# Kernel optimization log

Measured on AMD Instinct MI355X. Metric: run time of the kernel, lower is better.

The kernel has to match this reference:

```python
import jax, jax.numpy as jnp
import numpy as np

NA, NW, H = 20000, 100000, 128
DA, DW = 64, 128
E_CR, E_IN, E_CO = 400000, 600000, 300000


def _seg_softmax(logits, seg, n):
    m = jax.ops.segment_max(logits, seg, num_segments=n)
    e = jnp.exp(logits - m[seg])
    s = jax.ops.segment_sum(e, seg, num_segments=n)
    return e / (s[seg] + 1e-16)


def _gat(x_src, x_dst, edge, W, b, a_s, a_d):
    # PyG GATConv, heads=1, concat=False, shared lin for src/dst, add_self_loops=True
    n_src, n_dst = x_src.shape[0], x_dst.shape[0]
    loops = jnp.arange(min(n_src, n_dst), dtype=edge.dtype)
    src = jnp.concatenate([edge[0], loops])
    dst = jnp.concatenate([edge[1], loops])
    hs = x_src @ W            # [n_src, H]
    hd = x_dst @ W            # [n_dst, H]
    logit = jax.nn.leaky_relu((hs @ a_s)[src] + (hd @ a_d)[dst], 0.2)
    alpha = _seg_softmax(logit, dst, n_dst)          # softmax over in-neighborhoods
    out = jax.ops.segment_sum(alpha[:, None] * hs[src], dst, num_segments=n_dst)
    return out + b


def _mlp2(x, w1, b1, w2, b2):
    return jax.nn.relu(x @ w1 + b1) @ w2 + b2


def setup_inputs() -> dict:
    key = jax.random.key(0)
    ks = iter(jax.random.split(key, 40))

    def p(shape, scale=0.1):
        return jax.random.normal(next(ks), shape, jnp.float32) * scale

    def edges(n_src, n_dst, E):
        s = jax.random.randint(next(ks), (E,), 0, n_src, dtype=jnp.int32)
        d = jax.random.randint(next(ks), (E,), 0, n_dst, dtype=jnp.int32)
        d = jnp.where(s == d, (d + 1) % n_dst, d)  # keep input loop-free (PyG strips them)
        return jnp.stack([s, d])

    e_creates = edges(NA, NW, E_CR)
    inp = {
        'artist_feat': jax.random.normal(next(ks), (NA, DA), jnp.float32),
        'work_feat': jax.random.normal(next(ks), (NW, DW), jnp.float32),
        'a_w1': p((DA, H)), 'a_b1': jnp.zeros(H, jnp.float32),
        'a_w2': p((H, H)), 'a_b2': jnp.zeros(H, jnp.float32),
        'w_w1': p((DW, H)), 'w_b1': jnp.zeros(H, jnp.float32),
        'w_w2': p((H, H)), 'w_b2': jnp.zeros(H, jnp.float32),
        'cr_W': p((H, H)), 'cr_b': jnp.zeros(H, jnp.float32), 'cr_as': p((H,)), 'cr_ad': p((H,)),
        'in_W': p((H, H)), 'in_b': jnp.zeros(H, jnp.float32), 'in_as': p((H,)), 'in_ad': p((H,)),
        'co_W': p((H, H)), 'co_b': jnp.zeros(H, jnp.float32), 'co_as': p((H,)), 'co_ad': p((H,)),
        'p_w1': p((2 * H, 256)), 'p_b1': jnp.zeros(256, jnp.float32),
        'p_w2': p((256, 128)), 'p_b2': jnp.zeros(128, jnp.float32),
        'p_w3': p((128, 1)), 'p_b3': jnp.zeros(1, jnp.float32),
        'e_creates': e_creates,
        'e_created_by': jnp.flip(e_creates, axis=0),  # reverse relation [work, artist]
        'e_infl': edges(NW, NW, E_IN),
        'e_collab': edges(NA, NA, E_CO),
    }
    return inp


def reference(artist_feat, work_feat,
              a_w1, a_b1, a_w2, a_b2,
              w_w1, w_b1, w_w2, w_b2,
              cr_W, cr_b, cr_as, cr_ad,
              in_W, in_b, in_as, in_ad,
              co_W, co_b, co_as, co_ad,
              p_w1, p_b1, p_w2, p_b2, p_w3, p_b3,
              e_creates, e_created_by, e_infl, e_collab):
    ax = _mlp2(artist_feat, a_w1, a_b1, a_w2, a_b2)      # [NA, H]
    wx = _mlp2(work_feat, w_w1, w_b1, w_w2, w_b2)        # [NW, H]
    wx = jax.nn.elu(_gat(ax, wx, e_creates, cr_W, cr_b, cr_as, cr_ad))
    wx = jax.nn.elu(_gat(wx, wx, e_infl, in_W, in_b, in_as, in_ad))
    au = _gat(wx, ax, e_created_by, cr_W, cr_b, cr_as, cr_ad)  # no elu (matches source)
    ac = jax.nn.elu(_gat(au, au, e_collab, co_W, co_b, co_as, co_ad))
    comb = jnp.concatenate([au, ac], axis=1)             # [NA, 2H]
    h = jax.nn.relu(comb @ p_w1 + p_b1)                  # dropout is identity in eval
    h = jax.nn.relu(h @ p_w2 + p_b2)
    return (h @ p_w3 + p_b3).squeeze()
```

## Files before the change

### kernel.cpp

```cpp
#include <hip/hip_runtime.h>
#include <hip/hip_bf16.h>
#include <cstddef>

#define NA 20000
#define NW 100000
#define HH 128
#define DA 64
#define E_CR 400000
#define E_IN 600000
#define E_CO 300000

#define ROW1 0
#define ROW2 (NW)
#define ROW3 (2 * NW)
#define ROW4 (2 * NW + NA)
#define NTOT (2 * NW + 2 * NA)
#define CAPW 40
#define CAPA 88
#define NPREP (10 * 128 + 1)
#define GNB ((NA + 127) / 128)

typedef short v8s __attribute__((ext_vector_type(8)));
typedef float v4f __attribute__((ext_vector_type(4)));

constexpr int PSLOT = 2 * 128 * 264;

__device__ inline short f2bf(float x) {
    union { float f; unsigned u; } c; c.f = x;
    unsigned r = c.u + 0x7fff + ((c.u >> 16) & 1);
    return (short)(r >> 16);
}
__device__ inline float bf2f(short s) {
    union { unsigned u; float f; } c; c.u = ((unsigned)(unsigned short)s) << 16;
    return c.f;
}
__device__ inline float bfu2f(unsigned short s) {
    union { unsigned u; float f; } c; c.u = ((unsigned)s) << 16;
    return c.f;
}

__device__ inline void split8(const float* xv, v8s& h, v8s& l) {
#pragma unroll
    for (int p = 0; p < 4; ++p) {
        float2 xf; xf.x = xv[2 * p]; xf.y = xv[2 * p + 1];
        __hip_bfloat162 hb = __float22bfloat162_rn(xf);
        float2 hf = __bfloat1622float2(hb);
        float2 lf; lf.x = xf.x - hf.x; lf.y = xf.y - hf.y;
        __hip_bfloat162 lb = __float22bfloat162_rn(lf);
        union { __hip_bfloat162 b; short2 s; } uh, ul;
        uh.b = hb; ul.b = lb;
        h[2 * p] = uh.s.x; h[2 * p + 1] = uh.s.y;
        l[2 * p] = ul.s.x; l[2 * p + 1] = ul.s.y;
    }
}

struct AppChunk { const int* e; int E; int* pad; int cap; int* deg; };

__device__ inline void do_append(const AppChunk& ap, int bid) {
    int b0 = bid * 1024 + threadIdx.x;
    int s[4], d[4]; bool ok[4];
#pragma unroll
    for (int u = 0; u < 4; ++u) {
        int i = b0 + u * 256;
        ok[u] = i < ap.E;
        s[u] = 0; d[u] = 0;
        if (ok[u]) { s[u] = ap.e[i]; d[u] = ap.e[ap.E + i]; }
    }
    int p[4];
#pragma unroll
    for (int u = 0; u < 4; ++u) if (ok[u]) p[u] = atomicAdd(&ap.deg[d[u]], 1);
#pragma unroll
    for (int u = 0; u < 4; ++u)
        if (ok[u] && p[u] < ap.cap)
            ap.pad[(size_t)d[u] * ap.cap + p[u]] = s[u];
}

struct PrepDesc { const float* src; int ldw; int K; };
struct PrepArgs {
    PrepDesc d[10]; const float* wvW; const float* wvA; float* vd;
    const float* gX; const float* gB; float* gY; int gM;
};

__global__ __launch_bounds__(256) void k_prep_append(PrepArgs a, short* __restrict__ out,
                                                    AppChunk ap)
{
    __shared__ short Bs2[2 * 128 * 72];
    if (blockIdx.x >= NPREP + GNB) { do_append(ap, blockIdx.x - NPREP - GNB); return; }
    if (blockIdx.x >= NPREP) {
        int bid = blockIdx.x - NPREP;
        const int tid = threadIdx.x;
        const int wave = tid >> 6, lane = tid & 63;
        const int l15 = lane & 15, quad = lane >> 4;
        const int wrow = bid * 128 + wave * 32;
        for (int e = tid; e < 64 * 128; e += 256) {
            int n = e & 127, k = e >> 7;
            float x = a.d[0].src[(size_t)k * 128 + n];
            short h = f2bf(x);
            short l = f2bf(x - bf2f(h));
            Bs2[n * 72 + k] = h;
            Bs2[128 * 72 + n * 72 + k] = l;
        }
        v8s ah[2][2], al[2][2];
#pragma unroll
        for (int rf = 0; rf < 2; ++rf) {
            int r = wrow + rf * 16 + l15; if (r >= a.gM) r = a.gM - 1;
            const float* xp = a.gX + (size_t)r * DA + quad * 8;
#pragma unroll
            for (int kf = 0; kf < 2; ++kf) {
                float xv[8];
                *(float4*)&xv[0] = *(const float4*)(xp + kf * 32);
                *(float4*)&xv[4] = *(const float4*)(xp + kf * 32 + 4);
                split8(xv, ah[rf][kf], al[rf][kf]);
            }
        }
        __syncthreads();
        v4f acc[2][8];
#pragma unroll
        for (int rf = 0; rf < 2; ++rf)
#pragma unroll
            for (int cf = 0; cf < 8; ++cf) acc[rf][cf] = (v4f){0.f, 0.f, 0.f, 0.f};
#pragma unroll
        for (int kf = 0; kf < 2; ++kf) {
#pragma unroll
            for (int cf = 0; cf < 8; ++cf) {
                int coff = (cf * 16 + l15) * 72 + kf * 32 + quad * 8;
                v8s bh = *(const v8s*)&Bs2[coff];
                v8s bl = *(const v8s*)&Bs2[128 * 72 + coff];
#pragma unroll
                for (int rf = 0; rf < 2; ++rf) {
                    acc[rf][cf] = __builtin_amdgcn_mfma_f32_16x16x32_bf16(al[rf][kf], bh, acc[rf][cf], 0, 0, 0);
                    acc[rf][cf] = __builtin_amdgcn_mfma_f32_16x16x32_bf16(ah[rf][kf], bl, acc[rf][cf], 0, 0, 0);
                    acc[rf][cf] = __builtin_amdgcn_mfma_f32_16x16x32_bf16(ah[rf][kf], bh, acc[rf][cf], 0, 0, 0);
                }
            }
        }
        float bv[8];
#pragma unroll
        for (int cf = 0; cf < 8; ++cf) bv[cf] = a.gB[cf * 16 + l15];
#pragma unroll
        for (int rf = 0; rf < 2; ++rf) {
#pragma unroll
            for (int reg = 0; reg < 4; ++reg) {
                int r = wrow + rf * 16 + quad * 4 + reg;
                if (r >= a.gM) continue;
                float* yp = a.gY + (size_t)r * HH;
#pragma unroll
                for (int cf = 0; cf < 8; ++cf) {
                    float o = acc[rf][cf][reg] + bv[cf];
                    yp[cf * 16 + l15] = o > 0.f ? o : 0.f;
                }
            }
        }
        return;
    }
    if (blockIdx.x == NPREP - 1) {
        __shared__ float sa[HH];
        int t = threadIdx.x;
        if (t < HH) sa[t] = a.wvA[t];
        __syncthreads();
        if (t < HH) {
            float s = 0.f;
            for (int jj = 0; jj < HH; ++jj) s += a.wvW[(size_t)t * HH + jj] * sa[jj];
            a.vd[t] = s;
        }
        return;
    }
    int m = blockIdx.x >> 7;
    int e = (blockIdx.x & 127) * 256 + threadIdx.x;
    PrepDesc dd = a.d[m];
    int K = dd.K;
    int KP = (K <= 128) ? K + 8 : K;
    if (e >= K * 128) return;
    int n = e & 127, k = e >> 7;
    float x = dd.src[(size_t)k * dd.ldw + n];
    short h = f2bf(x);
    short l = f2bf(x - bf2f(h));
    short* base = out + (size_t)m * PSLOT;
    base[n * KP + k] = h;
    base[128 * KP + n * KP + k] = l;
}

template<int K, int ACT, int NSS, int ST, int LDSB, int OBF, int DUAL, int XBF>
__global__ __launch_bounds__(256, 2) void k_mfma(
    const float* __restrict__ X, int ldx,
    const short* __restrict__ Wp,
    const float* __restrict__ bias,
    float* __restrict__ Y, int ldy, int M,
    const float* __restrict__ v1, float* __restrict__ ss1,
    const float* __restrict__ v2, float* __restrict__ ss2,
    const float* __restrict__ sb)
{
    constexpr int KF = K / 32;
    constexpr int KP = LDSB ? K + 8 : K;
    __shared__ short Bs[LDSB ? 2 * 128 * (K + 8) : 8];
    const int tid = threadIdx.x;
    const int wave = tid >> 6, lane = tid & 63;
    const int l15 = lane & 15, quad = lane >> 4;
    int bid = blockIdx.x;
    if (DUAL) {
        int g0 = gridDim.x >> 1;
        if (bid >= g0) { bid -= g0; Wp += PSLOT; bias += 128; Y += 128; }
    }
    const int wrow = bid * 128 + wave * 32;

    if (LDSB) {
        const float4* src = (const float4*)Wp;
        float4* dst = (float4*)Bs;
        constexpr int total = 2 * 128 * KP / 8;
        for (int i = tid; i < total; i += 256) dst[i] = src[i];
    }

    v4f acc[2][8];
#pragma unroll
    for (int rf = 0; rf < 2; ++rf)
#pragma unroll
        for (int cf = 0; cf < 8; ++cf) acc[rf][cf] = (v4f){0.f, 0.f, 0.f, 0.f};

    v8s ah[2][KF], al[2][KF];
#pragma unroll
    for (int rf = 0; rf < 2; ++rf) {
        int r = wrow + rf * 16 + l15; if (r >= M) r = M - 1;
        if (XBF) {
            const unsigned short* xp = (const unsigned short*)X + (size_t)r * ldx + quad * 8;
#pragma unroll
            for (int kf = 0; kf < KF; ++kf)
                ah[rf][kf] = *(const v8s*)(xp + kf * 32);
        } else {
            const float* xp = X + (size_t)r * ldx + quad * 8;
#pragma unroll
            for (int kf = 0; kf < KF; ++kf) {
                float xv[8];
                *(float4*)&xv[0] = *(const float4*)(xp + kf * 32);
                *(float4*)&xv[4] = *(const float4*)(xp + kf * 32 + 4);
                split8(xv, ah[rf][kf], al[rf][kf]);
            }
        }
    }
    if (LDSB) __syncthreads();
#pragma unroll
    for (int kf = 0; kf < KF; ++kf) {
#pragma unroll
        for (int cf = 0; cf < 8; ++cf) {
            const short* bp = LDSB ? &Bs[(cf * 16 + l15) * KP + kf * 32 + quad * 8]
                                   : Wp + (size_t)(cf * 16 + l15) * K + kf * 32 + quad * 8;
            v8s bh = *(const v8s*)bp;
            v8s bl = *(const v8s*)(bp + 128 * KP);
#pragma unroll
            for (int rf = 0; rf < 2; ++rf) {
                if (!XBF) acc[rf][cf] = __builtin_amdgcn_mfma_f32_16x16x32_bf16(al[rf][kf], bh, acc[rf][cf], 0, 0, 0);
                acc[rf][cf] = __builtin_amdgcn_mfma_f32_16x16x32_bf16(ah[rf][kf], bl, acc[rf][cf], 0, 0, 0);
                acc[rf][cf] = __builtin_amdgcn_mfma_f32_16x16x32_bf16(ah[rf][kf], bh, acc[rf][cf], 0, 0, 0);
            }
        }
    }

    float bv[8], v1c[8], v2c[8];
#pragma unroll
    for (int cf = 0; cf < 8; ++cf) {
        int col = cf * 16 + l15;
        bv[cf] = bias ? bias[col] : 0.f;
        if (NSS >= 1) v1c[cf] = v1[col];
        if (NSS >= 2) v2c[cf] = v2[col];
    }
    float sbv = (NSS >= 1 && sb) ? sb[0] : 0.f;

#pragma unroll
    for (int rf = 0; rf < 2; ++rf) {
#pragma unroll
        for (int reg = 0; reg < 4; ++reg) {
            int r = wrow + rf * 16 + quad * 4 + reg;
            if (r >= M) continue;
            float p1 = 0.f, p2 = 0.f;
#pragma unroll
            for (int cf = 0; cf < 8; ++cf) {
                float o = acc[rf][cf][reg] + bv[cf];
                if (ACT == 1) o = o > 0.f ? o : 0.f;
                if (NSS >= 1) p1 = fmaf(o, v1c[cf], p1);
                if (NSS >= 2) p2 = fmaf(o, v2c[cf], p2);
                if (ST) {
                    if (OBF) ((unsigned short*)Y)[(size_t)r * ldy + cf * 16 + l15] = (unsigned short)f2bf(o);
                    else     Y[(size_t)r * ldy + cf * 16 + l15] = o;
                }
            }
            if (NSS >= 1) {
#pragma unroll
                for (int w = 1; w < 16; w <<= 1) {
                    p1 += __shfl_xor(p1, w, 64);
                    if (NSS >= 2) p2 += __shfl_xor(p2, w, 64);
                }
                if (l15 == 0) {
                    ss1[r] = p1 + sbv;
                    if (NSS >= 2) ss2[r] = p2;
                }
            }
        }
    }
}

struct MfmaCfg {
    const float* X; int ldx;
    const short* Wp;
    const float* bias;
    float* Y; int ldy; int M;
    int act, nss, obf, xbf, st;
    const float* v1; float* ss1;
    const float* v2; float* ss2;
    int nblocks;
};

__global__ __launch_bounds__(256, 2) void k_mfma2(MfmaCfg c0, MfmaCfg c1, AppChunk ap)
{
    constexpr int KF = 4, KP = 136;
    __shared__ short Bs[2 * 128 * KP];
    int bid = blockIdx.x;
    if (bid >= c0.nblocks + c1.nblocks) { do_append(ap, bid - c0.nblocks - c1.nblocks); return; }
    const bool first = bid < c0.nblocks;
    const MfmaCfg& c = first ? c0 : c1;
    if (!first) bid -= c0.nblocks;
    const int tid = threadIdx.x;
    const int wave = tid >> 6, lane = tid & 63;
    const int l15 = lane & 15, quad = lane >> 4;
    const int wrow = bid * 128 + wave * 32;

    {
        const float4* src = (const float4*)c.Wp;
        float4* dst = (float4*)Bs;
        constexpr int total = 2 * 128 * KP / 8;
        for (int i = tid; i < total; i += 256) dst[i] = src[i];
    }

    v4f acc[2][8];
#pragma unroll
    for (int rf = 0; rf < 2; ++rf)
#pragma unroll
        for (int cf = 0; cf < 8; ++cf) acc[rf][cf] = (v4f){0.f, 0.f, 0.f, 0.f};

    v8s ah[2][KF], al[2][KF];
#pragma unroll
    for (int rf = 0; rf < 2; ++rf) {
        int r = wrow + rf * 16 + l15; if (r >= c.M) r = c.M - 1;
        if (c.xbf) {
            const unsigned short* xp = (const unsigned short*)c.X + (size_t)r * c.ldx + quad * 8;
#pragma unroll
            for (int kf = 0; kf < KF; ++kf) {
                ah[rf][kf] = *(const v8s*)(xp + kf * 32);
                al[rf][kf] = (v8s)(short)0;
            }
        } else {
            const float* xp = c.X + (size_t)r * c.ldx + quad * 8;
#pragma unroll
            for (int kf = 0; kf < KF; ++kf) {
                float xv[8];
                *(float4*)&xv[0] = *(const float4*)(xp + kf * 32);
                *(float4*)&xv[4] = *(const float4*)(xp + kf * 32 + 4);
                split8(xv, ah[rf][kf], al[rf][kf]);
            }
        }
    }
    __syncthreads();
#pragma unroll
    for (int kf = 0; kf < KF; ++kf) {
#pragma unroll
        for (int cf = 0; cf < 8; ++cf) {
            const short* bp = &Bs[(cf * 16 + l15) * KP + kf * 32 + quad * 8];
            v8s bh = *(const v8s*)bp;
            v8s bl = *(const v8s*)(bp + 128 * KP);
#pragma unroll
            for (int rf = 0; rf < 2; ++rf) {
                if (!c.xbf) acc[rf][cf] = __builtin_amdgcn_mfma_f32_16x16x32_bf16(al[rf][kf], bh, acc[rf][cf], 0, 0, 0);
                acc[rf][cf] = __builtin_amdgcn_mfma_f32_16x16x32_bf16(ah[rf][kf], bl, acc[rf][cf], 0, 0, 0);
                acc[rf][cf] = __builtin_amdgcn_mfma_f32_16x16x32_bf16(ah[rf][kf], bh, acc[rf][cf], 0, 0, 0);
            }
        }
    }

    float bv[8], v1c[8], v2c[8];
#pragma unroll
    for (int cf = 0; cf < 8; ++cf) {
        int col = cf * 16 + l15;
        bv[cf] = c.bias ? c.bias[col] : 0.f;
        v1c[cf] = (c.nss >= 1) ? c.v1[col] : 0.f;
        v2c[cf] = (c.nss >= 2) ? c.v2[col] : 0.f;
    }

#pragma unroll
    for (int rf = 0; rf < 2; ++rf) {
#pragma unroll
        for (int reg = 0; reg < 4; ++reg) {
            int r = wrow + rf * 16 + quad * 4 + reg;
            if (r >= c.M) continue;
            float p1 = 0.f, p2 = 0.f;
#pragma unroll
            for (int cf = 0; cf < 8; ++cf) {
                float o = acc[rf][cf][reg] + bv[cf];
                if (c.act) o = o > 0.f ? o : 0.f;
                p1 = fmaf(o, v1c[cf], p1);
                p2 = fmaf(o, v2c[cf], p2);
                if (c.st) {
                    if (c.obf) ((unsigned short*)c.Y)[(size_t)r * c.ldy + cf * 16 + l15] = (unsigned short)f2bf(o);
                    else       c.Y[(size_t)r * c.ldy + cf * 16 + l15] = o;
                }
            }
            if (c.nss >= 1) {
#pragma unroll
                for (int w = 1; w < 16; w <<= 1) {
                    p1 += __shfl_xor(p1, w, 64);
                    p2 += __shfl_xor(p2, w, 64);
                }
                if (l15 == 0) {
                    c.ss1[r] = p1;
                    if (c.nss >= 2) c.ss2[r] = p2;
                }
            }
        }
    }
}

template<int ELU, int U, int CAP, int OBF>
__global__ __launch_bounds__(256) void k_aggregate(
    const int* __restrict__ deg, const int* __restrict__ esp,
    const unsigned short* __restrict__ hs, const float* __restrict__ ss,
    const float* __restrict__ sd, const float* __restrict__ bias,
    void* __restrict__ out, int ldy, int n, int loopn)
{
    int lane = threadIdx.x & 63;
    int wv = threadIdx.x >> 6;
    int d = blockIdx.x * 4 + wv;
    if (d >= n) return;
    int half = lane >> 5;
    int col = (lane & 31) * 4;
    const int* row = esp + (size_t)d * CAP;
    int i1 = deg[d]; if (i1 > CAP) i1 = CAP;
    float sdv = sd[d];
    float den = 0.f;
    float ax = 0.f, ay = 0.f, az = 0.f, aw = 0.f;
    if (half == 0 && d < loopn) {
        ushort4 h = *(const ushort4*)(hs + (size_t)d * HH + col);
        float l = ss[d] + sdv;
        l = l < 0.f ? 0.2f * l : l;
        float e = __expf(l);
        den += e;
        ax = fmaf(e, bfu2f(h.x), ax);
        ay = fmaf(e, bfu2f(h.y), ay);
        az = fmaf(e, bfu2f(h.z), az);
        aw = fmaf(e, bfu2f(h.w), aw);
    }
    int i = 0;
    for (; i + 2 * U <= i1; i += 2 * U) {
        int s[U]; ushort4 h[U]; float sv[U];
#pragma unroll
        for (int u = 0; u < U; ++u) s[u] = row[i + 2 * u + half];
#pragma unroll
        for (int u = 0; u < U; ++u) h[u] = *(const ushort4*)(hs + (size_t)s[u] * HH + col);
#pragma unroll
        for (int u = 0; u < U; ++u) sv[u] = ss[s[u]];
#pragma unroll
        for (int u = 0; u < U; ++u) {
            float l = sv[u] + sdv;
            l = l < 0.f ? 0.2f * l : l;
            float e = __expf(l);
            den += e;
            ax = fmaf(e, bfu2f(h[u].x), ax);
            ay = fmaf(e, bfu2f(h[u].y), ay);
            az = fmaf(e, bfu2f(h[u].z), az);
            aw = fmaf(e, bfu2f(h[u].w), aw);
        }
    }
    if (i < i1) {
        int s[U]; ushort4 h[U]; float sv[U]; bool act[U];
#pragma unroll
        for (int u = 0; u < U; ++u) {
            int idx = i + 2 * u + half;
            act[u] = idx < i1;
            s[u] = row[act[u] ? idx : (i1 - 1)];
        }
#pragma unroll
        for (int u = 0; u < U; ++u) h[u] = *(const ushort4*)(hs + (size_t)s[u] * HH + col);
#pragma unroll
        for (int u = 0; u < U; ++u) sv[u] = ss[s[u]];
#pragma unroll
        for (int u = 0; u < U; ++u) {
            float l = sv[u] + sdv;
            l = l < 0.f ? 0.2f * l : l;
            float e = act[u] ? __expf(l) : 0.f;
            den += e;
            ax = fmaf(e, bfu2f(h[u].x), ax);
            ay = fmaf(e, bfu2f(h[u].y), ay);
            az = fmaf(e, bfu2f(h[u].z), az);
            aw = fmaf(e, bfu2f(h[u].w), aw);
        }
    }
    den += __shfl_xor(den, 32, 64);
    ax += __shfl_xor(ax, 32, 64);
    ay += __shfl_xor(ay, 32, 64);
    az += __shfl_xor(az, 32, 64);
    aw += __shfl_xor(aw, 32, 64);
    if (half == 0) {
        float4 b = *(const float4*)(bias + col);
        float inv = 1.f / (den + 1e-16f);
        float o0 = ax * inv + b.x;
        float o1 = ay * inv + b.y;
        float o2 = az * inv + b.z;
        float o3 = aw * inv + b.w;
        if (ELU) {
            o0 = o0 > 0.f ? o0 : expm1f(o0);
            o1 = o1 > 0.f ? o1 : expm1f(o1);
            o2 = o2 > 0.f ? o2 : expm1f(o2);
            o3 = o3 > 0.f ? o3 : expm1f(o3);
        }
        if (OBF) {
            ushort4 ob;
            ob.x = (unsigned short)f2bf(o0);
            ob.y = (unsigned short)f2bf(o1);
            ob.z = (unsigned short)f2bf(o2);
            ob.w = (unsigned short)f2bf(o3);
            *(ushort4*)((unsigned short*)out + (size_t)d * ldy + col) = ob;
        } else {
            *(float4*)((float*)out + (size_t)d * ldy + col) = make_float4(o0, o1, o2, o3);
        }
    }
}

extern "C" void kernel_launch(void* const* d_in, const int* in_sizes, int n_in,
                              void* d_out, int out_size, void* d_ws, size_t ws_size,
                              hipStream_t stream)
{
    const float* artist = (const float*)d_in[0];
    const float* workf  = (const float*)d_in[1];
    const float* a_w1 = (const float*)d_in[2];  const float* a_b1 = (const float*)d_in[3];
    const float* a_w2 = (const float*)d_in[4];  const float* a_b2 = (const float*)d_in[5];
    const float* w_w1 = (const float*)d_in[6];  const float* w_b1 = (const float*)d_in[7];
    const float* w_w2 = (const float*)d_in[8];  const float* w_b2 = (const float*)d_in[9];
    const float* cr_W = (const float*)d_in[10]; const float* cr_b = (const float*)d_in[11];
    const float* cr_as = (const float*)d_in[12]; const float* cr_ad = (const float*)d_in[13];
    const float* in_W = (const float*)d_in[14]; const float* in_b = (const float*)d_in[15];
    const float* in_as = (const float*)d_in[16]; const float* in_ad = (const float*)d_in[17];
    const float* co_W = (const float*)d_in[18]; const float* co_b = (const float*)d_in[19];
    const float* co_as = (const float*)d_in[20]; const float* co_ad = (const float*)d_in[21];
    const float* p_w1 = (const float*)d_in[22]; const float* p_b1 = (const float*)d_in[23];
    const float* p_w2 = (const float*)d_in[24]; const float* p_b2 = (const float*)d_in[25];
    const float* p_w3 = (const float*)d_in[26]; const float* p_b3 = (const float*)d_in[27];
    const int* e_cr = (const int*)d_in[28];
    const int* e_cb = (const int*)d_in[29];
    const int* e_in = (const int*)d_in[30];
    const int* e_co = (const int*)d_in[31];

    char* wsp = (char*)d_ws;
    size_t off = 0;
    auto alloc = [&](size_t bytes) -> void* {
        void* p = wsp + off;
        off += (bytes + 255) / 256 * 256;
        return p;
    };
    float* ax   = (float*)alloc((size_t)NA * HH * 4);
    float* hsA  = (float*)alloc((size_t)NA * HH * 4);
    unsigned short* hsw = (unsigned short*)alloc((size_t)NW * HH * 2);
    unsigned short* wxb = (unsigned short*)alloc((size_t)NW * HH * 2);
    unsigned short* hsb = (unsigned short*)alloc((size_t)NW * HH * 2);
    float* h1   = (float*)alloc((size_t)NA * 256 * 4);
    float* comb = (float*)alloc((size_t)NA * 256 * 4);
    float* ss1 = (float*)alloc((size_t)NA * 4);
    float* sd1 = (float*)alloc((size_t)NW * 4);
    float* ss2 = (float*)alloc((size_t)NW * 4);
    float* sd2 = (float*)alloc((size_t)NW * 4);
    float* ss3 = (float*)alloc((size_t)NW * 4);
    float* sd3 = (float*)alloc((size_t)NA * 4);
    float* ss4 = (float*)alloc((size_t)NA * 4);
    float* sd4 = (float*)alloc((size_t)NA * 4);
    float* vd  = (float*)alloc(HH * 4);
    int* deg   = (int*)alloc((size_t)NTOT * 4);
    int* pad1  = (int*)alloc((size_t)NW * CAPW * 4);
    int* pad2  = (int*)alloc((size_t)NW * CAPW * 4);
    int* pad3  = (int*)alloc((size_t)NA * CAPA * 4);
    int* pad4  = (int*)alloc((size_t)NA * CAPA * 4);
    short* preW = (short*)alloc((size_t)10 * PSLOT * 2);
    (void)ws_size; (void)in_sizes; (void)n_in; (void)out_size;

    auto pre = [&](int m) { return preW + (size_t)m * PSLOT; };
    auto gg = [](int M) { return (M + 127) / 128; };
    auto apb = [](int E) { return (E + 1023) / 1024; };
    const float* nf = nullptr;
    float* nfm = nullptr;

    PrepArgs pa;
    pa.d[0] = {a_w1, HH, DA};
    pa.d[1] = {a_w2, HH, HH};
    pa.d[2] = {w_w1, HH, HH};
    pa.d[3] = {w_w2, HH, HH};
    pa.d[4] = {cr_W, HH, HH};
    pa.d[5] = {in_W, HH, HH};
    pa.d[6] = {co_W, HH, HH};
    pa.d[7] = {p_w1, 256, 256};
    pa.d[8] = {p_w1 + 128, 256, 256};
    pa.d[9] = {p_w2, HH, 256};
    pa.wvW = cr_W; pa.wvA = cr_ad; pa.vd = vd;
    pa.gX = artist; pa.gB = a_b1; pa.gY = hsA; pa.gM = NA;

    AppChunk ap1 = {e_cr, E_CR, pad1, CAPW, deg + ROW1};
    AppChunk ap2 = {e_in, E_IN, pad2, CAPW, deg + ROW2};
    AppChunk ap3 = {e_cb, E_CR, pad3, CAPA, deg + ROW3};
    AppChunk ap4 = {e_co, E_CO, pad4, CAPA, deg + ROW4};

    (void)hipMemsetAsync(deg, 0, (size_t)NTOT * 4, stream);

    k_prep_append<<<NPREP + GNB + apb(E_CR), 256, 0, stream>>>(pa, preW, ap1);

    {
        MfmaCfg c0 = {workf, HH, pre(2), w_b1, (float*)hsw, HH, NW, 1, 0, 1, 0, 1, nf, nfm, nf, nfm, gg(NW)};
        MfmaCfg c1 = {hsA, HH, pre(1), a_b2, ax, HH, NA, 0, 1, 0, 0, 1, vd, sd3, nf, nfm, gg(NA)};
        k_mfma2<<<gg(NW) + gg(NA) + apb(E_IN), 256, 0, stream>>>(c0, c1, ap2);
    }
    {
        MfmaCfg c0 = {(const float*)hsw, HH, pre(3), w_b2, nfm, HH, NW, 0, 1, 0, 1, 0, vd, sd1, nf, nfm, gg(NW)};
        MfmaCfg c1 = {ax, HH, pre(4), nullptr, (float*)hsb, HH, NA, 0, 1, 1, 0, 1, cr_as, ss1, nf, nfm, gg(NA)};
        k_mfma2<<<gg(NW) + gg(NA) + apb(E_CR), 256, 0, stream>>>(c0, c1, ap3);
    }

    k_aggregate<1, 2, CAPW, 1><<<(NW + 3) / 4, 256, 0, stream>>>(deg + ROW1, pad1, hsb, ss1, sd1, cr_b, wxb, HH, NW, NA);

    {
        MfmaCfg c0 = {(const float*)wxb, HH, pre(5), nullptr, (float*)hsb, HH, NW, 0, 2, 1, 1, 1, in_as, ss2, in_ad, sd2, gg(NW)};
        MfmaCfg c1 = {nullptr, 0, nullptr, nullptr, nullptr, 0, 0, 0, 0, 0, 0, 0, nf, nfm, nf, nfm, 0};
        k_mfma2<<<gg(NW) + apb(E_CO), 256, 0, stream>>>(c0, c1, ap4);
    }
    k_aggregate<1, 2, CAPW, 1><<<(NW + 3) / 4, 256, 0, stream>>>(deg + ROW2, pad2, hsb, ss2, sd2, in_b, wxb, HH, NW, NW);

    k_mfma<HH, 0, 1, 1, 1, 1, 0, 1><<<gg(NW), 256, 0, stream>>>((const float*)wxb, HH, pre(4), nullptr, (float*)hsb, HH, NW, cr_as, ss3, nf, nfm, nf);
    k_aggregate<0, 4, CAPA, 0><<<(NA + 3) / 4, 256, 0, stream>>>(deg + ROW3, pad3, hsb, ss3, sd3, cr_b, comb, 256, NA, NA);

    k_mfma<HH, 0, 2, 1, 1, 1, 0, 0><<<gg(NA), 256, 0, stream>>>(comb, 256, pre(6), nullptr, (float*)hsb, HH, NA, co_as, ss4, co_ad, sd4, nf);
    k_aggregate<1, 4, CAPA, 0><<<(NA + 3) / 4, 256, 0, stream>>>(deg + ROW4, pad4, hsb, ss4, sd4, co_b, comb + 128, 256, NA, NA);

    k_mfma<256, 1, 0, 1, 0, 0, 1, 0><<<2 * gg(NA), 256, 0, stream>>>(comb, 256, pre(7), p_b1, h1, 256, NA, nf, nfm, nf, nfm, nf);
    k_mfma<256, 1, 1, 0, 0, 0, 0, 0><<<gg(NA), 256, 0, stream>>>(h1, 256, pre(9), p_b2, nfm, 0, NA, p_w3, (float*)d_out, nf, nfm, p_b3);
}
```

Before: 577.5 us.

## Read GEMM weights from global instead of LDS and raise occupancy to four blocks

The MFMA kernels stop staging the split bf16 weights in shared memory and read them straight from global/L2. X fragments are now loaded per k-step instead of all at once, which cuts register pressure, and launch bounds go from 2 to 4 blocks per CU. Edge-append blocks are moved to the front of the fused grids so the long atomic work starts first. In exchange, weight reads may hit cache less well than LDS and put more pressure on L2 bandwidth.

```diff
diff --git a/kernel.cpp b/kernel.cpp
--- a/kernel.cpp
+++ b/kernel.cpp
@@ -85,9 +85,12 @@
                                                     AppChunk ap)
 {
     __shared__ short Bs2[2 * 128 * 72];
-    if (blockIdx.x >= NPREP + GNB) { do_append(ap, blockIdx.x - NPREP - GNB); return; }
-    if (blockIdx.x >= NPREP) {
-        int bid = blockIdx.x - NPREP;
+    const int napp = (ap.E + 1023) >> 10;
+    int bx = blockIdx.x;
+    if (bx < napp) { do_append(ap, bx); return; }
+    bx -= napp;
+    if (bx < GNB) {
+        const int bid = bx;
         const int tid = threadIdx.x;
         const int wave = tid >> 6, lane = tid & 63;
         const int l15 = lane & 15, quad = lane >> 4;
@@ -153,7 +156,8 @@
         }
         return;
     }
-    if (blockIdx.x == NPREP - 1) {
+    bx -= GNB;
+    if (bx == NPREP - 1) {
         __shared__ float sa[HH];
         int t = threadIdx.x;
         if (t < HH) sa[t] = a.wvA[t];
@@ -165,8 +169,8 @@
         }
         return;
     }
-    int m = blockIdx.x >> 7;
-    int e = (blockIdx.x & 127) * 256 + threadIdx.x;
+    int m = bx >> 7;
+    int e = (bx & 127) * 256 + threadIdx.x;
     PrepDesc dd = a.d[m];
     int K = dd.K;
     int KP = (K <= 128) ? K + 8 : K;
@@ -181,7 +185,7 @@
 }
 
 template<int K, int ACT, int NSS, int ST, int LDSB, int OBF, int DUAL, int XBF>
-__global__ __launch_bounds__(256, 2) void k_mfma(
+__global__ __launch_bounds__(256, 4) void k_mfma(
     const float* __restrict__ X, int ldx,
     const short* __restrict__ Wp,
     const float* __restrict__ bias,
@@ -191,8 +195,8 @@
     const float* __restrict__ sb)
 {
     constexpr int KF = K / 32;
-    constexpr int KP = LDSB ? K + 8 : K;
-    __shared__ short Bs[LDSB ? 2 * 128 * (K + 8) : 8];
+    constexpr int KP = (K <= 128) ? K + 8 : K;
+    __shared__ short Bs[LDSB ? 2 * 128 * KP : 8];
     const int tid = threadIdx.x;
     const int wave = tid >> 6, lane = tid & 63;
     const int l15 = lane & 15, quad = lane >> 4;
@@ -208,6 +212,7 @@
         float4* dst = (float4*)Bs;
         constexpr int total = 2 * 128 * KP / 8;
         for (int i = tid; i < total; i += 256) dst[i] = src[i];
+        __syncthreads();
     }
 
     v4f acc[2][8];
@@ -216,40 +221,40 @@
 #pragma unroll
         for (int cf = 0; cf < 8; ++cf) acc[rf][cf] = (v4f){0.f, 0.f, 0.f, 0.f};
 
-    v8s ah[2][KF], al[2][KF];
+    const unsigned short* xb16[2];
+    const float* xb32[2];
 #pragma unroll
     for (int rf = 0; rf < 2; ++rf) {
         int r = wrow + rf * 16 + l15; if (r >= M) r = M - 1;
-        if (XBF) {
-            const unsigned short* xp = (const unsigned short*)X + (size_t)r * ldx + quad * 8;
-#pragma unroll
-            for (int kf = 0; kf < KF; ++kf)
-                ah[rf][kf] = *(const v8s*)(xp + kf * 32);
-        } else {
-            const float* xp = X + (size_t)r * ldx + quad * 8;
-#pragma unroll
-            for (int kf = 0; kf < KF; ++kf) {
+        xb16[rf] = (const unsigned short*)X + (size_t)r * ldx + quad * 8;
+        xb32[rf] = X + (size_t)r * ldx + quad * 8;
+    }
+
+#pragma unroll
+    for (int kf = 0; kf < KF; ++kf) {
+        v8s ah[2], al[2];
+#pragma unroll
+        for (int rf = 0; rf < 2; ++rf) {
+            if (XBF) {
+                ah[rf] = *(const v8s*)(xb16[rf] + kf * 32);
+            } else {
                 float xv[8];
-                *(float4*)&xv[0] = *(const float4*)(xp + kf * 32);
-                *(float4*)&xv[4] = *(const float4*)(xp + kf * 32 + 4);
-                split8(xv, ah[rf][kf], al[rf][kf]);
-            }
-        }
-    }
-    if (LDSB) __syncthreads();
-#pragma unroll
-    for (int kf = 0; kf < KF; ++kf) {
+                *(float4*)&xv[0] = *(const float4*)(xb32[rf] + kf * 32);
+                *(float4*)&xv[4] = *(const float4*)(xb32[rf] + kf * 32 + 4);
+                split8(xv, ah[rf], al[rf]);
+            }
+        }
 #pragma unroll
         for (int cf = 0; cf < 8; ++cf) {
             const short* bp = LDSB ? &Bs[(cf * 16 + l15) * KP + kf * 32 + quad * 8]
-                                   : Wp + (size_t)(cf * 16 + l15) * K + kf * 32 + quad * 8;
+                                   : Wp + (size_t)(cf * 16 + l15) * KP + kf * 32 + quad * 8;
             v8s bh = *(const v8s*)bp;
             v8s bl = *(const v8s*)(bp + 128 * KP);
 #pragma unroll
             for (int rf = 0; rf < 2; ++rf) {
-                if (!XBF) acc[rf][cf] = __builtin_amdgcn_mfma_f32_16x16x32_bf16(al[rf][kf], bh, acc[rf][cf], 0, 0, 0);
-                acc[rf][cf] = __builtin_amdgcn_mfma_f32_16x16x32_bf16(ah[rf][kf], bl, acc[rf][cf], 0, 0, 0);
-                acc[rf][cf] = __builtin_amdgcn_mfma_f32_16x16x32_bf16(ah[rf][kf], bh, acc[rf][cf], 0, 0, 0);
+                if (!XBF) acc[rf][cf] = __builtin_amdgcn_mfma_f32_16x16x32_bf16(al[rf], bh, acc[rf][cf], 0, 0, 0);
+                acc[rf][cf] = __builtin_amdgcn_mfma_f32_16x16x32_bf16(ah[rf], bl, acc[rf][cf], 0, 0, 0);
+                acc[rf][cf] = __builtin_amdgcn_mfma_f32_16x16x32_bf16(ah[rf], bh, acc[rf][cf], 0, 0, 0);
             }
         }
     }
@@ -308,12 +313,13 @@
     int nblocks;
 };
 
-__global__ __launch_bounds__(256, 2) void k_mfma2(MfmaCfg c0, MfmaCfg c1, AppChunk ap)
+__global__ __launch_bounds__(256, 4) void k_mfma2(MfmaCfg c0, MfmaCfg c1, AppChunk ap)
 {
     constexpr int KF = 4, KP = 136;
-    __shared__ short Bs[2 * 128 * KP];
+    const int napp = (ap.E + 1023) >> 10;
     int bid = blockIdx.x;
-    if (bid >= c0.nblocks + c1.nblocks) { do_append(ap, bid - c0.nblocks - c1.nblocks); return; }
+    if (bid < napp) { do_append(ap, bid); return; }
+    bid -= napp;
     const bool first = bid < c0.nblocks;
     const MfmaCfg& c = first ? c0 : c1;
     if (!first) bid -= c0.nblocks;
@@ -322,54 +328,46 @@
     const int l15 = lane & 15, quad = lane >> 4;
     const int wrow = bid * 128 + wave * 32;
 
-    {
-        const float4* src = (const float4*)c.Wp;
-        float4* dst = (float4*)Bs;
-        constexpr int total = 2 * 128 * KP / 8;
-        for (int i = tid; i < total; i += 256) dst[i] = src[i];
-    }
-
     v4f acc[2][8];
 #pragma unroll
     for (int rf = 0; rf < 2; ++rf)
 #pragma unroll
         for (int cf = 0; cf < 8; ++cf) acc[rf][cf] = (v4f){0.f, 0.f, 0.f, 0.f};
 
-    v8s ah[2][KF], al[2][KF];
+    const unsigned short* xb16[2];
+    const float* xb32[2];
 #pragma unroll
     for (int rf = 0; rf < 2; ++rf) {
         int r = wrow + rf * 16 + l15; if (r >= c.M) r = c.M - 1;
-        if (c.xbf) {
-            const unsigned short* xp = (const unsigned short*)c.X + (size_t)r * c.ldx + quad * 8;
-#pragma unroll
-            for (int kf = 0; kf < KF; ++kf) {
-                ah[rf][kf] = *(const v8s*)(xp + kf * 32);
-                al[rf][kf] = (v8s)(short)0;
-            }
-        } else {
-            const float* xp = c.X + (size_t)r * c.ldx + quad * 8;
-#pragma unroll
-            for (int kf = 0; kf < KF; ++kf) {
+        xb16[rf] = (const unsigned short*)c.X + (size_t)r * c.ldx + quad * 8;
+        xb32[rf] = c.X + (size_t)r * c.ldx + quad * 8;
+    }
+
+#pragma unroll
+    for (int kf = 0; kf < KF; ++kf) {
+        v8s ah[2], al[2];
+#pragma unroll
+        for (int rf = 0; rf < 2; ++rf) {
+            if (c.xbf) {
+                ah[rf] = *(const v8s*)(xb16[rf] + kf * 32);
+                al[rf] = (v8s)(short)0;
+            } else {
                 float xv[8];
-                *(float4*)&xv[0] = *(const float4*)(xp + kf * 32);
-                *(float4*)&xv[4] = *(const float4*)(xp + kf * 32 + 4);
-                split8(xv, ah[rf][kf], al[rf][kf]);
-            }
-        }
-    }
-    __syncthreads();
-#pragma unroll
-    for (int kf = 0; kf < KF; ++kf) {
+                *(float4*)&xv[0] = *(const float4*)(xb32[rf] + kf * 32);
+                *(float4*)&xv[4] = *(const float4*)(xb32[rf] + kf * 32 + 4);
+                split8(xv, ah[rf], al[rf]);
+            }
+        }
 #pragma unroll
         for (int cf = 0; cf < 8; ++cf) {
-            const short* bp = &Bs[(cf * 16 + l15) * KP + kf * 32 + quad * 8];
+            const short* bp = c.Wp + (size_t)(cf * 16 + l15) * KP + kf * 32 + quad * 8;
             v8s bh = *(const v8s*)bp;
             v8s bl = *(const v8s*)(bp + 128 * KP);
 #pragma unroll
             for (int rf = 0; rf < 2; ++rf) {
-                if (!c.xbf) acc[rf][cf] = __builtin_amdgcn_mfma_f32_16x16x32_bf16(al[rf][kf], bh, acc[rf][cf], 0, 0, 0);
-                acc[rf][cf] = __builtin_amdgcn_mfma_f32_16x16x32_bf16(ah[rf][kf], bl, acc[rf][cf], 0, 0, 0);
-                acc[rf][cf] = __builtin_amdgcn_mfma_f32_16x16x32_bf16(ah[rf][kf], bh, acc[rf][cf], 0, 0, 0);
+                if (!c.xbf) acc[rf][cf] = __builtin_amdgcn_mfma_f32_16x16x32_bf16(al[rf], bh, acc[rf][cf], 0, 0, 0);
+                acc[rf][cf] = __builtin_amdgcn_mfma_f32_16x16x32_bf16(ah[rf], bl, acc[rf][cf], 0, 0, 0);
+                acc[rf][cf] = __builtin_amdgcn_mfma_f32_16x16x32_bf16(ah[rf], bh, acc[rf][cf], 0, 0, 0);
             }
         }
     }
@@ -625,10 +623,10 @@
     }
     k_aggregate<1, 2, CAPW, 1><<<(NW + 3) / 4, 256, 0, stream>>>(deg + ROW2, pad2, hsb, ss2, sd2, in_b, wxb, HH, NW, NW);
 
-    k_mfma<HH, 0, 1, 1, 1, 1, 0, 1><<<gg(NW), 256, 0, stream>>>((const float*)wxb, HH, pre(4), nullptr, (float*)hsb, HH, NW, cr_as, ss3, nf, nfm, nf);
+    k_mfma<HH, 0, 1, 1, 0, 1, 0, 1><<<gg(NW), 256, 0, stream>>>((const float*)wxb, HH, pre(4), nullptr, (float*)hsb, HH, NW, cr_as, ss3, nf, nfm, nf);
     k_aggregate<0, 4, CAPA, 0><<<(NA + 3) / 4, 256, 0, stream>>>(deg + ROW3, pad3, hsb, ss3, sd3, cr_b, comb, 256, NA, NA);
 
-    k_mfma<HH, 0, 2, 1, 1, 1, 0, 0><<<gg(NA), 256, 0, stream>>>(comb, 256, pre(6), nullptr, (float*)hsb, HH, NA, co_as, ss4, co_ad, sd4, nf);
+    k_mfma<HH, 0, 2, 1, 0, 1, 0, 0><<<gg(NA), 256, 0, stream>>>(comb, 256, pre(6), nullptr, (float*)hsb, HH, NA, co_as, ss4, co_ad, sd4, nf);
     k_aggregate<1, 4, CAPA, 0><<<(NA + 3) / 4, 256, 0, stream>>>(deg + ROW4, pad4, hsb, ss4, sd4, co_b, comb + 128, 256, NA, NA);
 
     k_mfma<256, 1, 0, 1, 0, 0, 1, 0><<<2 * gg(NA), 256, 0, stream>>>(comb, 256, pre(7), p_b1, h1, 256, NA, nf, nfm, nf, nfm, nf);
```

After: 589.6 us. +2.1%, slower.
